# Kernel optimization log

Measured on AMD Instinct MI355X. Metric: run time of the kernel, lower is better.

The kernel has to match this reference:

```python
import jax, jax.numpy as jnp
import numpy as np
import math

P = 2; GS = 64; TPS = 32; T = TPS * TPS; DIM = 256; NH = 8; HD = DIM // NH; NL = 5; FFH = 1024
SCALES = ((0.15, 16), (0.3, 32))
ENC_H = 32; ENC_O = 64
XMIN, XMAX, YMIN, YMAX = -2.0, 4.0, -1.5, 1.5
NFREQ = 10
N_PTS = 20000; N_Q = 100000; G = GS * GS


def rope_tables():
    half = HD // 2
    inv = 1.0 / (10000.0 ** (jnp.arange(0, half, 2, dtype=jnp.float32) / half))  # [HD/4]
    h = jnp.arange(TPS, dtype=jnp.float32)
    w = jnp.arange(TPS, dtype=jnp.float32)
    hg, wg = jnp.meshgrid(h, w, indexing='ij')
    ax = wg.reshape(-1)[:, None] * inv[None, :]  # [T, HD/4]
    ay = hg.reshape(-1)[:, None] * inv[None, :]
    return jnp.cos(ax), jnp.sin(ax), jnp.cos(ay), jnp.sin(ay)


def apply_rope(x, cx, sx, cy, sy):
    B, H, Tn, D = x.shape
    hd = D // 2; pd = hd // 2
    xp = x[..., :hd].reshape(B, H, Tn, pd, 2)
    yp = x[..., hd:].reshape(B, H, Tn, pd, 2)
    cx = cx[None, None]; sx = sx[None, None]; cy = cy[None, None]; sy = sy[None, None]
    rx = jnp.stack([xp[..., 0] * cx - xp[..., 1] * sx, xp[..., 0] * sx + xp[..., 1] * cx], -1).reshape(B, H, Tn, hd)
    ry = jnp.stack([yp[..., 0] * cy - yp[..., 1] * sy, yp[..., 0] * sy + yp[..., 1] * cy], -1).reshape(B, H, Tn, hd)
    return jnp.concatenate([rx, ry], -1)


def rmsnorm(x, w):
    n = jax.lax.rsqrt(jnp.mean(x.astype(jnp.float32) ** 2, -1, keepdims=True) + 1e-6)
    return (x.astype(jnp.float32) * n).astype(x.dtype) * w


def encode_scale(grid, points, radius, k, w1, b1, w2, b2):
    # squared distances [G, N] via gemm (monotone in euclidean dist -> same topk)
    g2 = jnp.sum(grid ** 2, -1, keepdims=True)
    p2 = jnp.sum(points ** 2, -1)
    d2 = g2 + p2[None, :] - 2.0 * (grid @ points.T)
    neg, idx = jax.lax.top_k(-d2, k)  # k nearest
    valid = (-neg) < radius * radius  # [G, k]
    rel = points[idx] - grid[:, None, :]  # [G, k, 2]
    rel = jnp.where(valid[..., None], rel, 0.0)
    h = jax.nn.relu(rel @ w1 + b1)
    f = h @ w2 + b2  # [G, k, ENC_O]
    masked = jnp.where(valid[..., None], f, -jnp.inf)
    pooled = jnp.max(masked, axis=1)
    return jnp.where(jnp.any(valid, axis=1)[:, None], pooled, 0.0)


def fourier_feats(x):
    freqs = (2.0 ** jnp.arange(NFREQ, dtype=jnp.float32)) * math.pi
    scaled = x[..., None] * freqs  # [..., 2, NFREQ]
    enc = jnp.concatenate([jnp.sin(scaled), jnp.cos(scaled)], -1).reshape(*x.shape[:-1], -1)
    return jnp.concatenate([x, enc], -1)  # [..., 2*(1+2*NFREQ)]


def bilinear_sample(feat, xn, yn):
    # feat [C,H,W]; xn,yn in [-1,1]; align_corners=True, border padding
    C, H, W = feat.shape
    px = (xn + 1.0) * 0.5 * (W - 1)
    py = (yn + 1.0) * 0.5 * (H - 1)
    x0 = jnp.clip(jnp.floor(px), 0, W - 1)
    y0 = jnp.clip(jnp.floor(py), 0, H - 1)
    wx = px - x0; wy = py - y0
    x0i = x0.astype(jnp.int32); y0i = y0.astype(jnp.int32)
    x1i = jnp.clip(x0i + 1, 0, W - 1); y1i = jnp.clip(y0i + 1, 0, H - 1)
    f00 = feat[:, y0i, x0i]; f01 = feat[:, y0i, x1i]
    f10 = feat[:, y1i, x0i]; f11 = feat[:, y1i, x1i]
    out = (f00 * (1 - wx) * (1 - wy) + f01 * wx * (1 - wy) + f10 * (1 - wx) * wy + f11 * wx * wy)
    return out.T  # [N, C]


def forward(points, grid, query_pos, query_uinf, query_sdf, query_sdf_grad,
            enc_w1, enc_b1, enc_w2, enc_b2, inproj_w, inproj_b, patch_w, patch_b,
            norm1_w, qkv_w, attnproj_w, norm2_w, gate_w, value_w, ffnout_w,
            unpatch_w, unpatch_b, posmlp_w1, posmlp_b1, posmlp_w2, posmlp_b2,
            pred_w1, pred_b1, pred_w2, pred_b2):
    # --- PointNet multi-scale encoder onto grid ---
    feats = [encode_scale(grid, points, SCALES[i][0], SCALES[i][1],
                          enc_w1[i], enc_b1[i], enc_w2[i], enc_b2[i]) for i in range(len(SCALES))]
    gfeat = jnp.concatenate(feats, -1) @ inproj_w + inproj_b  # [G, DIM]
    img = gfeat.reshape(GS, GS, DIM).transpose(2, 0, 1)[None]  # [1, DIM, GS, GS]
    # --- patchify ---
    x = img.reshape(1, DIM, TPS, P, TPS, P).transpose(0, 2, 4, 1, 3, 5).reshape(1, T, DIM * P * P)
    tok = x @ patch_w + patch_b  # [1, T, DIM]
    cx, sx, cy, sy = rope_tables()
    scale = 1.0 / math.sqrt(HD)
    for l in range(NL):
        h = rmsnorm(tok, norm1_w[l])
        qkv = (h @ qkv_w[l]).reshape(1, T, 3, NH, HD).transpose(2, 0, 3, 1, 4)
        q, k, v = qkv[0], qkv[1], qkv[2]
        q = apply_rope(q, cx, sx, cy, sy)
        k = apply_rope(k, cx, sx, cy, sy)
        att = jax.nn.softmax(jnp.einsum('bhqd,bhkd->bhqk', q, k) * scale, axis=-1)
        o = jnp.einsum('bhqk,bhkd->bhqd', att, v).transpose(0, 2, 1, 3).reshape(1, T, DIM)
        tok = tok + o @ attnproj_w[l]
        h2 = rmsnorm(tok, norm2_w[l])
        tok = tok + (jax.nn.silu(h2 @ gate_w[l]) * (h2 @ value_w[l])) @ ffnout_w[l]
    up = tok @ unpatch_w + unpatch_b  # [1, T, DIM*P*P]
    proc = up.reshape(1, TPS, TPS, DIM, P, P).transpose(0, 3, 1, 4, 2, 5).reshape(1, DIM, GS, GS)
    # --- decoder ---
    xn = jnp.clip(2.0 * (query_pos[:, 0] - XMIN) / (XMAX - XMIN) - 1.0, -1.0, 1.0)
    yn = jnp.clip(2.0 * (query_pos[:, 1] - YMIN) / (YMAX - YMIN) - 1.0, -1.0, 1.0)
    local = bilinear_sample(proc[0], xn, yn)  # [Nq, DIM]
    fp = fourier_feats(jnp.stack([xn, yn], -1))  # [Nq, 42]
    other = jnp.concatenate([query_uinf, query_sdf, query_sdf_grad], -1)  # [Nq, 5]
    pin = jnp.concatenate([fp, other], -1)  # [Nq, 47]
    pe = jax.nn.relu(pin @ posmlp_w1 + posmlp_b1) @ posmlp_w2 + posmlp_b2  # [Nq, 512]
    ctx = jnp.concatenate([local, pe], -1)  # [Nq, 768]
    return jax.nn.relu(ctx @ pred_w1 + pred_b1) @ pred_w2 + pred_b2  # [Nq, 4]


def setup_inputs() -> dict:
    key = jax.random.key(0)
    ks = jax.random.split(key, 32)
    def lin(k, fi, fo, stack=None):
        sh = (fi, fo) if stack is None else (stack, fi, fo)
        return jax.random.normal(k, sh, jnp.float32) / np.sqrt(fi)
    ux = jax.random.uniform(ks[0], (N_PTS, 2), jnp.float32)
    points = jnp.stack([XMIN + ux[:, 0] * (XMAX - XMIN), YMIN + ux[:, 1] * (YMAX - YMIN)], -1)
    gx = jnp.linspace(XMIN, XMAX, GS); gy = jnp.linspace(YMIN, YMAX, GS)
    gyy, gxx = jnp.meshgrid(gy, gx, indexing='ij')
    grid = jnp.stack([gxx.reshape(-1), gyy.reshape(-1)], -1).astype(jnp.float32)  # row-major (H,W)
    uq = jax.random.uniform(ks[1], (N_Q, 2), jnp.float32)
    query_pos = jnp.stack([XMIN + uq[:, 0] * (XMAX - XMIN), YMIN + uq[:, 1] * (YMAX - YMIN)], -1)
    nsc = len(SCALES); pf = DIM * P * P; cdim = 2 * (1 + 2 * NFREQ) + 5
    return {
        'points': points, 'grid': grid, 'query_pos': query_pos,
        'query_uinf': jax.random.normal(ks[2], (N_Q, 2), jnp.float32),
        'query_sdf': jax.random.normal(ks[3], (N_Q, 1), jnp.float32),
        'query_sdf_grad': jax.random.normal(ks[4], (N_Q, 2), jnp.float32),
        'enc_w1': lin(ks[5], 2, ENC_H, nsc), 'enc_b1': jnp.zeros((nsc, ENC_H), jnp.float32),
        'enc_w2': lin(ks[6], ENC_H, ENC_O, nsc), 'enc_b2': jnp.zeros((nsc, ENC_O), jnp.float32),
        'inproj_w': lin(ks[7], ENC_O * nsc, DIM), 'inproj_b': jnp.zeros((DIM,), jnp.float32),
        'patch_w': lin(ks[8], pf, DIM), 'patch_b': jnp.zeros((DIM,), jnp.float32),
        'norm1_w': jnp.ones((NL, DIM), jnp.float32),
        'qkv_w': lin(ks[9], DIM, 3 * DIM, NL),
        'attnproj_w': lin(ks[10], DIM, DIM, NL),
        'norm2_w': jnp.ones((NL, DIM), jnp.float32),
        'gate_w': lin(ks[11], DIM, FFH, NL),
        'value_w': lin(ks[12], DIM, FFH, NL),
        'ffnout_w': lin(ks[13], FFH, DIM, NL),
        'unpatch_w': lin(ks[14], DIM, pf), 'unpatch_b': jnp.zeros((pf,), jnp.float32),
        'posmlp_w1': lin(ks[15], cdim, 256), 'posmlp_b1': jnp.zeros((256,), jnp.float32),
        'posmlp_w2': lin(ks[16], 256, 512), 'posmlp_b2': jnp.zeros((512,), jnp.float32),
        'pred_w1': lin(ks[17], DIM + 512, 256), 'pred_b1': jnp.zeros((256,), jnp.float32),
        'pred_w2': lin(ks[18], 256, 4), 'pred_b2': jnp.zeros((4,), jnp.float32),
    }


def reference(points, grid, query_pos, query_uinf, query_sdf, query_sdf_grad,
              enc_w1, enc_b1, enc_w2, enc_b2, inproj_w, inproj_b, patch_w, patch_b,
              norm1_w, qkv_w, attnproj_w, norm2_w, gate_w, value_w, ffnout_w,
              unpatch_w, unpatch_b, posmlp_w1, posmlp_b1, posmlp_w2, posmlp_b2,
              pred_w1, pred_b1, pred_w2, pred_b2):
    return forward(points, grid, query_pos, query_uinf, query_sdf, query_sdf_grad,
                   enc_w1, enc_b1, enc_w2, enc_b2, inproj_w, inproj_b, patch_w, patch_b,
                   norm1_w, qkv_w, attnproj_w, norm2_w, gate_w, value_w, ffnout_w,
                   unpatch_w, unpatch_b, posmlp_w1, posmlp_b1, posmlp_w2, posmlp_b2,
                   pred_w1, pred_b1, pred_w2, pred_b2)
```

## Files before the change

### kernel.cpp

```cpp
#include <hip/hip_runtime.h>
#include <math.h>

typedef __attribute__((ext_vector_type(8))) short short8;
typedef __attribute__((ext_vector_type(8))) unsigned short ushort8;
typedef __attribute__((ext_vector_type(4))) unsigned short ushort4v;
typedef __attribute__((ext_vector_type(4))) float f32x4;
typedef __attribute__((ext_vector_type(16))) float f32x16;

#define NPTS  20000
#define NQ    100000
#define TOK   1024
#define DIMD  256
#define NHD   8
#define NLAY  5
#define GRD   4096
#define CAP   512
#define QN    32

#define XMINF (-2.0f)
#define YMINF (-1.5f)
#define CELL  0.15f
#define NCX   40
#define NCY   20
#define NCELL 800
// ... 133 lines not shown
    if (pi < nsel) {
      float rx = s_selx[pi] - gx;
      float ry = s_sely[pi] - gy;
      float f = B2[d];
      #pragma unroll
      for (int j = 0; j < 32; ++j) {
        float h = rx * W1[j] + ry * W1[32 + j] + B1[j];
        h = fmaxf(h, 0.0f);
        f += h * W2[j*64 + d];
      }
      s_part[grp][d] = fmaxf(s_part[grp][d], f);
    }
  }
  __syncthreads();
  if (tid < 64) {
    float v = fmaxf(fmaxf(s_part[0][tid], s_part[1][tid]),
                    fmaxf(s_part[2][tid], s_part[3][tid]));
    if (nsel == 0) v = 0.0f;
    ushort h, l; split2(v, h, l);
    fH[gi*128 + sc*64 + tid] = h;
    fL[gi*128 + sc*64 + tid] = l;
  }
}

__global__ void k_gemm(const float* __restrict__ A, const float* __restrict__ B,
                       float* __restrict__ C, int M, int N, int K) {
  __shared__ float As[32][33];
  __shared__ float Bs[32][33];
  int bm = blockIdx.y * 32, bn = blockIdx.x * 32;
  int tx = threadIdx.x & 31, ty = threadIdx.x >> 5;
  float acc[4] = {0.f, 0.f, 0.f, 0.f};
  for (int k0 = 0; k0 < K; k0 += 32) {
    for (int i = threadIdx.x; i < 1024; i += 256) {
      int r = i >> 5, c = i & 31;
      As[r][c] = A[(size_t)(bm + r)*K + k0 + c];
      Bs[r][c] = B[(size_t)(k0 + r)*N + bn + c];
    }
    __syncthreads();
    #pragma unroll
    for (int kk = 0; kk < 32; ++kk) {
      float bv = Bs[kk][tx];
      #pragma unroll
      for (int i = 0; i < 4; ++i) acc[i] += As[ty + 8*i][kk] * bv;
    }
    __syncthreads();
  }
  #pragma unroll
  for (int i = 0; i < 4; ++i)
    C[(size_t)(bm + ty + 8*i)*N + bn + tx] = acc[i];
}

__global__ void k_beff(const float* __restrict__ db1, const float* __restrict__ pb2,
                       const float* __restrict__ dw1, float* __restrict__ b2eff) {
  int n = threadIdx.x;
  float a = db1[n];
  for (int j = 0; j < 512; ++j) a += pb2[j] * dw1[(size_t)(256 + j)*256 + n];
  b2eff[n] = a;
}

struct SDesc { const float* src; ushort* dh; ushort* dl; int K, N, Kp, blk0; };
struct STable { int nw; SDesc d[31]; };

__global__ void k_splitT_all(STable tab) {
  __shared__ float tile[32][33];
  int b = blockIdx.x;
  int w = 0;
  for (int i = 1; i < tab.nw; ++i) if (b >= tab.d[i].blk0) w = i;
  SDesc s = tab.d[w];
  int rel = b - s.blk0;
  int ntn = s.N >> 5;
  int tk = rel / ntn, tn = rel - tk*ntn;
  int r = threadIdx.x >> 5, c = threadIdx.x & 31;
  #pragma unroll
  for (int i = 0; i < 4; ++i) {
    int kk = tk*32 + r + i*8;
    tile[r + i*8][c] = (kk < s.K) ? s.src[(size_t)kk*s.N + tn*32 + c] : 0.f;
  }
  __syncthreads();
  #pragma unroll
  for (int i = 0; i < 4; ++i) {
    int nn = tn*32 + r + i*8;
    float v = tile[c][r + i*8];
    ushort hh, ll; split2(v, hh, ll);
    size_t o = (size_t)nn*s.Kp + tk*32 + c;
    s.dh[o] = hh; s.dl[o] = ll;
  }
}

template<bool BIAS, bool RESID, bool WSPLIT>
__global__ __launch_bounds__(256,2)
void k_mgemm64(const ushort* __restrict__ Ah, const ushort* __restrict__ Al,
               const ushort* __restrict__ Bh, const ushort* __restrict__ Bl,
               const float* __restrict__ bias, const float* __restrict__ resid,
               float* __restrict__ C, int M, int N, int K,
               ushort* __restrict__ wsH, ushort* __restrict__ wsL) {
  __shared__ ushort sAh[64*40], sAl[64*40], sBh[64*40], sBl[64*40];
  int tid = threadIdx.x;
  int wave = tid >> 6, lane = tid & 63, l15 = lane & 15, lhi = lane >> 4;
  int bm = blockIdx.y * 64, bn = blockIdx.x * 64;
  int sr = tid >> 2, sg = (tid & 3) * 8;
  const size_t aoff = (size_t)(bm + sr) * K + sg;
  const size_t boff = (size_t)(bn + sr) * K + sg;
  f32x4 acc[4];
  #pragma unroll
  for (int m = 0; m < 4; ++m) acc[m] = (f32x4){0.f,0.f,0.f,0.f};

  for (int k0 = 0; k0 < K; k0 += 32) {
    __syncthreads();
    *(ushort8*)(sAh + sr*40 + sg) = *(const ushort8*)(Ah + aoff + k0);
    *(ushort8*)(sAl + sr*40 + sg) = *(const ushort8*)(Al + aoff + k0);
// ... 110 lines not shown
  int sr = tid >> 2, sg = (tid & 3) * 8;
  const int K = 256;
  const size_t aoff = (size_t)(bm + sr) * K + sg;
  const size_t boff = (size_t)(bn + sr) * K + sg;
  f32x4 acc[4];
  #pragma unroll
  for (int m = 0; m < 4; ++m) acc[m] = (f32x4){0.f,0.f,0.f,0.f};

  for (int k0 = 0; k0 < K; k0 += 32) {
    __syncthreads();
    *(ushort8*)(sAh + sr*40 + sg) = *(const ushort8*)(Ah + aoff + k0);
    *(ushort8*)(sAl + sr*40 + sg) = *(const ushort8*)(Al + aoff + k0);
    *(ushort8*)(sBh + sr*40 + sg) = *(const ushort8*)(Bh + boff + k0);
    *(ushort8*)(sBl + sr*40 + sg) = *(const ushort8*)(Bl + boff + k0);
    __syncthreads();
    short8 ah[4], al[4];
    #pragma unroll
    for (int m = 0; m < 4; ++m) {
      int r = m*16 + l15;
      ah[m] = *(const short8*)(sAh + r*40 + lhi*8);
      al[m] = *(const short8*)(sAl + r*40 + lhi*8);
    }
    int rb = wave*16 + l15;
    short8 bh = *(const short8*)(sBh + rb*40 + lhi*8);
    short8 bl = *(const short8*)(sBl + rb*40 + lhi*8);
    #pragma unroll
    for (int m = 0; m < 4; ++m) {
      acc[m] = MFMA(ah[m], bh, acc[m]);
      acc[m] = MFMA(al[m], bh, acc[m]);
      acc[m] = MFMA(ah[m], bl, acc[m]);
    }
  }

  int u = bn + wave*16 + l15;
  float bv = bias[u];
  int c  = u >> 2;
  int py = (u >> 1) & 1, px = u & 1;
  #pragma unroll
  for (int m = 0; m < 4; ++m) {
    int gr0 = bm + m*16 + lhi*4;
    #pragma unroll
    for (int r = 0; r < 4; ++r) {
      int t = gr0 + r;
      int y = (t >> 5)*2 + py, x = (t & 31)*2 + px;
      float v = acc[m][r] + bv;
      ushort hh, ll; split2(v, hh, ll);
      size_t o = (size_t)(y*64 + x)*256 + c;
      pH[o] = hh; pL[o] = ll;
    }
  }
}

__global__ __launch_bounds__(256,2)
void k_qkvrope(const ushort* __restrict__ Ah, const ushort* __restrict__ Al,
               const ushort* __restrict__ Bh, const ushort* __restrict__ Bl,
               ushort* __restrict__ QsH, ushort* __restrict__ QsL,
               ushort* __restrict__ KsH, ushort* __restrict__ KsL,
               ushort* __restrict__ VtH, ushort* __restrict__ VtL) {
  __shared__ ushort sAh[64*40], sAl[64*40], sBh[64*40], sBl[64*40];
  int tid = threadIdx.x;
  int wave = tid >> 6, lane = tid & 63, l15 = lane & 15, lhi = lane >> 4;
  int bm = blockIdx.y * 64, bn = blockIdx.x * 64;
  int sr = tid >> 2, sg = (tid & 3) * 8;
  const int K = 256, N = 768;
  const size_t aoff = (size_t)(bm + sr) * K + sg;
  const size_t boff = (size_t)(bn + sr) * K + sg;
  f32x4 acc[4];
  #pragma unroll
  for (int m = 0; m < 4; ++m) acc[m] = (f32x4){0.f,0.f,0.f,0.f};
  (void)N;

  for (int k0 = 0; k0 < K; k0 += 32) {
    __syncthreads();
    *(ushort8*)(sAh + sr*40 + sg) = *(const ushort8*)(Ah + aoff + k0);
    *(ushort8*)(sAl + sr*40 + sg) = *(const ushort8*)(Al + aoff + k0);
    *(ushort8*)(sBh + sr*40 + sg) = *(const ushort8*)(Bh + boff + k0);
    *(ushort8*)(sBl + sr*40 + sg) = *(const ushort8*)(Bl + boff + k0);
    __syncthreads();
    short8 ah[4], al[4];
    #pragma unroll
    for (int m = 0; m < 4; ++m) {
      int r = m*16 + l15;
      ah[m] = *(const short8*)(sAh + r*40 + lhi*8);
      al[m] = *(const short8*)(sAl + r*40 + lhi*8);
    }
    int rb = wave*16 + l15;
    short8 bh = *(const short8*)(sBh + rb*40 + lhi*8);
    short8 bl = *(const short8*)(sBl + rb*40 + lhi*8);
    #pragma unroll
    for (int m = 0; m < 4; ++m) {
      acc[m] = MFMA(ah[m], bh, acc[m]);
      acc[m] = MFMA(al[m], bh, acc[m]);
      acc[m] = MFMA(ah[m], bl, acc[m]);
    }
  }

  int gc = bn + wave*16 + l15;
  if (gc < 512) {
    int qk = gc >> 8;
    int c  = gc & 255;
    int h  = c >> 5, d = c & 31;
    int half = d >> 4, dd = d & 15, pd = dd >> 1, odd = dd & 1;
    float inv = powf(10.0f, -0.5f * (float)pd);
    float scl = qk ? 1.0f : 0.17677669529663687f;
    ushort* dH = qk ? KsH : QsH;
    ushort* dL = qk ? KsL : QsL;
    #pragma unroll
    for (int m = 0; m < 4; ++m) {
      int gr0 = bm + m*16 + lhi*4;
      #pragma unroll
      for (int r = 0; r < 4; ++r) {
        int t = gr0 + r;
        float v = acc[m][r];
        float pv = __shfl_xor(v, 1);
        float pos = (float)(half ? (t >> 5) : (t & 31));
        float ang = pos * inv;
        float cs = __cosf(ang), sn = __sinf(ang);
        float res = odd ? (pv*sn + v*cs) : (v*cs - pv*sn);
        res *= scl;
        ushort hh, ll; split2(res, hh, ll);
        size_t o = (size_t)h*32768 + (size_t)t*32 + d;
        dH[o] = hh; dL[o] = ll;
      }
    }
  } else {
    int c = gc - 512;
    int h = c >> 5, d = c & 31;
    #pragma unroll
    for (int m = 0; m < 4; ++m) {
      int t0 = bm + m*16 + lhi*4;
      ushort4v vh, vl;
      #pragma unroll
      for (int r = 0; r < 4; ++r) {
        ushort hh, ll; split2(acc[m][r], hh, ll);
        vh[r] = hh; vl[r] = ll;
      }
      size_t o = (size_t)h*32768 + (size_t)d*1024 + t0;
      *(ushort4v*)(VtH + o) = vh;
      *(ushort4v*)(VtL + o) = vl;
    }
  }
}

__global__ void k_rmsnorm_split(const float* __restrict__ x, const float* __restrict__ w,
                                ushort* __restrict__ yH, ushort* __restrict__ yL) {
  __shared__ float red[256];
  int row = blockIdx.x, t = threadIdx.x;
  float v = x[(size_t)row*DIMD + t];
  red[t] = v * v;
  __syncthreads();
  for (int off = 128; off; off >>= 1) {
    if (t < off) red[t] += red[t + off];
    __syncthreads();
  }
  float n = 1.0f / sqrtf(red[0] / 256.0f + 1e-6f);
  float y = v * n * w[t];
  ushort h, l; split2(y, h, l);
  yH[(size_t)row*DIMD + t] = h;
  yL[(size_t)row*DIMD + t] = l;
}

__global__ __launch_bounds__(512,1)
void k_fattn(const ushort* __restrict__ QsH, const ushort* __restrict__ QsL,
             const ushort* __restrict__ KsH, const ushort* __restrict__ KsL,
             const ushort* __restrict__ VtH, const ushort* __restrict__ VtL,
             ushort* __restrict__ oH, ushort* __restrict__ oL) {
  __shared__ float sM[8][64], sL[8][64];
  __shared__ float sO[8][64][16];
  int h  = blockIdx.x >> 5;
  int qt = blockIdx.x & 31;
  int tid = threadIdx.x;
  int wv = tid >> 6, lane = tid & 63;
  int l31 = lane & 31, lhi = (lane >> 5) & 1;

  const size_t qoff = ((size_t)h*1024 + qt*32 + l31)*32 + lhi*8;
  short8 qh = *(const short8*)(QsH + qoff);
  short8 ql = *(const short8*)(QsL + qoff);

  f32x16 oacc;
  #pragma unroll
  for (int r = 0; r < 16; ++r) oacc[r] = 0.f;
  float mrun = -INFINITY, lrun = 0.f;

  for (int kt = wv*4; kt < wv*4 + 4; ++kt) {
    const size_t koff = ((size_t)h*1024 + kt*32 + l31)*32 + lhi*8;
    short8 kh = *(const short8*)(KsH + koff);
    short8 kl = *(const short8*)(KsL + koff);
    const size_t voff = ((size_t)h*32 + l31)*1024 + kt*32 + lhi*8;
    short8 vh0 = *(const short8*)(VtH + voff);
    short8 vl0 = *(const short8*)(VtL + voff);
    short8 vh1 = *(const short8*)(VtH + voff + 16);
    short8 vl1 = *(const short8*)(VtL + voff + 16);

    f32x16 s;
    #pragma unroll
    for (int r = 0; r < 16; ++r) s[r] = 0.f;
    s = MFMA32(kh, qh, s);
    s = MFMA32(kl, qh, s);
    s = MFMA32(kh, ql, s);

    float mloc = s[0];
    #pragma unroll
    for (int r = 1; r < 16; ++r) mloc = fmaxf(mloc, s[r]);
    mloc = fmaxf(mloc, __shfl_xor(mloc, 32));
    float mnew = fmaxf(mrun, mloc);
    float fsc = __expf(mrun - mnew);
    float p[16]; float ssum = 0.f;
    #pragma unroll
    for (int r = 0; r < 16; ++r) { p[r] = __expf(s[r] - mnew); ssum += p[r]; }
    ssum += __shfl_xor(ssum, 32);
    lrun = lrun * fsc + ssum;
    mrun = mnew;
    #pragma unroll
    for (int r = 0; r < 16; ++r) oacc[r] *= fsc;
// ... 17 lines not shown
    U bh0, bl0, bh1, bl1;
    bh0.u[0] = lhi ? pwh[2] : wh[0];  bh0.u[1] = lhi ? pwh[3] : wh[1];
    bh0.u[2] = lhi ? wh[2]  : pwh[0]; bh0.u[3] = lhi ? wh[3]  : pwh[1];
    bl0.u[0] = lhi ? pwl[2] : wl[0];  bl0.u[1] = lhi ? pwl[3] : wl[1];
    bl0.u[2] = lhi ? wl[2]  : pwl[0]; bl0.u[3] = lhi ? wl[3]  : pwl[1];
    bh1.u[0] = lhi ? pwh[6] : wh[4];  bh1.u[1] = lhi ? pwh[7] : wh[5];
    bh1.u[2] = lhi ? wh[6]  : pwh[4]; bh1.u[3] = lhi ? wh[7]  : pwh[5];
    bl1.u[0] = lhi ? pwl[6] : wl[4];  bl1.u[1] = lhi ? pwl[7] : wl[5];
    bl1.u[2] = lhi ? wl[6]  : pwl[4]; bl1.u[3] = lhi ? wl[7]  : pwl[5];

    oacc = MFMA32(vh0, bh0.s, oacc);
    oacc = MFMA32(vl0, bh0.s, oacc);
    oacc = MFMA32(vh0, bl0.s, oacc);
    oacc = MFMA32(vh1, bh1.s, oacc);
    oacc = MFMA32(vl1, bh1.s, oacc);
    oacc = MFMA32(vh1, bl1.s, oacc);
  }

  sM[wv][lane] = mrun;
  sL[wv][lane] = lrun;
  #pragma unroll
  for (int r = 0; r < 16; ++r) sO[wv][lane][r] = oacc[r];
  __syncthreads();

  if (wv == 0) {
    float M = sM[0][lane];
    #pragma unroll
    for (int w = 1; w < 8; ++w) M = fmaxf(M, sM[w][lane]);
    float L = 0.f;
    float O[16];
    #pragma unroll
    for (int r = 0; r < 16; ++r) O[r] = 0.f;
    #pragma unroll
    for (int w = 0; w < 8; ++w) {
      float f = __expf(sM[w][lane] - M);
      L += sL[w][lane] * f;
      #pragma unroll
      for (int r = 0; r < 16; ++r) O[r] += sO[w][lane][r] * f;
    }
    float inv = 1.0f / L;
    int t = qt*32 + l31;
    #pragma unroll
    for (int r = 0; r < 16; ++r) {
      int d = (r & 3) + 8*(r >> 2) + 4*lhi;
      float v = O[r] * inv;
      ushort hh, ll; split2(v, hh, ll);
      oH[(size_t)t*DIMD + h*32 + d] = hh;
      oL[(size_t)t*DIMD + h*32 + d] = ll;
    }
  }
}

__global__ __launch_bounds__(256,2)
void k_ffgv(const ushort* __restrict__ Ah, const ushort* __restrict__ Al,
            const ushort* __restrict__ Bh, const ushort* __restrict__ Bl,
            ushort* __restrict__ fH, ushort* __restrict__ fL) {
  __shared__ ushort sAh[64*40], sAl[64*40];
  __shared__ ushort sGh[64*40], sGl[64*40];
  __shared__ ushort sVh[64*40], sVl[64*40];
  int tid = threadIdx.x;
  int wave = tid >> 6, lane = tid & 63, l15 = lane & 15, lhi = lane >> 4;
  int bm = blockIdx.y * 64, bn = blockIdx.x * 64;
  int sr = tid >> 2, sg = (tid & 3) * 8;
  const size_t aoff = (size_t)(bm + sr) * 256 + sg;
  const size_t goff = (size_t)(bn + sr) * 256 + sg;
  const size_t voff = (size_t)(1024 + bn + sr) * 256 + sg;
  f32x4 accg[4], accv[4];
  #pragma unroll
  for (int m = 0; m < 4; ++m) { accg[m] = (f32x4){0.f,0.f,0.f,0.f}; accv[m] = accg[m]; }

  for (int k0 = 0; k0 < 256; k0 += 32) {
    __syncthreads();
    *(ushort8*)(sAh + sr*40 + sg) = *(const ushort8*)(Ah + aoff + k0);
    *(ushort8*)(sAl + sr*40 + sg) = *(const ushort8*)(Al + aoff + k0);
    *(ushort8*)(sGh + sr*40 + sg) = *(const ushort8*)(Bh + goff + k0);
    *(ushort8*)(sGl + sr*40 + sg) = *(const ushort8*)(Bl + goff + k0);
    *(ushort8*)(sVh + sr*40 + sg) = *(const ushort8*)(Bh + voff + k0);
    *(ushort8*)(sVl + sr*40 + sg) = *(const ushort8*)(Bl + voff + k0);
    __syncthreads();
    short8 ah[4], al[4];
    #pragma unroll
    for (int m = 0; m < 4; ++m) {
      int r = m*16 + l15;
      ah[m] = *(const short8*)(sAh + r*40 + lhi*8);
      al[m] = *(const short8*)(sAl + r*40 + lhi*8);
    }
    int rb = wave*16 + l15;
    short8 gh = *(const short8*)(sGh + rb*40 + lhi*8);
    short8 gl = *(const short8*)(sGl + rb*40 + lhi*8);
    short8 vh = *(const short8*)(sVh + rb*40 + lhi*8);
    short8 vl = *(const short8*)(sVl + rb*40 + lhi*8);
    #pragma unroll
    for (int m = 0; m < 4; ++m) {
      accg[m] = MFMA(ah[m], gh, accg[m]);
      accg[m] = MFMA(al[m], gh, accg[m]);
      accg[m] = MFMA(ah[m], gl, accg[m]);
      accv[m] = MFMA(ah[m], vh, accv[m]);
      accv[m] = MFMA(al[m], vh, accv[m]);
      accv[m] = MFMA(ah[m], vl, accv[m]);
    }
  }

  int gc = bn + wave*16 + l15;
  #pragma unroll
  for (int m = 0; m < 4; ++m) {
    int gr0 = bm + m*16 + lhi*4;
    #pragma unroll
    for (int r = 0; r < 4; ++r) {
      float g = accg[m][r], v = accv[m][r];
      float s = g / (1.0f + expf(-g));
      float rr = s * v;
      ushort hh, ll; split2(rr, hh, ll);
      size_t idx = (size_t)(gr0 + r)*1024 + gc;
      fH[idx] = hh; fL[idx] = ll;
    }
  }
}

__global__ __launch_bounds__(512,4)
void k_qhead(const float* __restrict__ qpos, const float* __restrict__ quinf,
             const float* __restrict__ qsdf, const float* __restrict__ qgrad,
             const float* __restrict__ projCL,
             const ushort* __restrict__ pw1tH, const ushort* __restrict__ pw1tL,
             const float* __restrict__ pb1,
             const ushort* __restrict__ wcH, const ushort* __restrict__ wcL,
             const float* __restrict__ b2eff,
             const float* __restrict__ dw2, const float* __restrict__ db2,
             float* __restrict__ out) {
  __shared__ ushort sPinH[QN*72], sPinL[QN*72];
  __shared__ ushort sH1H[QN*264], sH1L[QN*264];
  __shared__ float  sXY[QN][2];
  __shared__ float  sRed[8][128];

  int tid = threadIdx.x;
  int w = tid >> 6, lane = tid & 63, l15 = lane & 15, lhi = lane >> 4;
  int q0 = blockIdx.x * QN;

  if (tid < QN) {
    int qg = q0 + tid;
    float x = qpos[(size_t)qg*2 + 0], y = qpos[(size_t)qg*2 + 1];
    float xn = fminf(fmaxf(2.0f*(x + 2.0f)/6.0f - 1.0f, -1.0f), 1.0f);
    float yn = fminf(fmaxf(2.0f*(y + 1.5f)/3.0f - 1.0f, -1.0f), 1.0f);
    sXY[tid][0] = xn; sXY[tid][1] = yn;
  }
  __syncthreads();

  {
    int q = tid >> 4;
    int j0 = (tid & 15) * 4;
    int qg = q0 + q;
    float xn = sXY[q][0], yn = sXY[q][1];
    #pragma unroll
    for (int jj = 0; jj < 4; ++jj) {
      int j = j0 + jj;
      float v = 0.f;
      if (j == 0) v = xn;
      else if (j == 1) v = yn;
      else if (j < 42) {
        int z = j - 2;
        int coord = z / 20;
        int ww = z % 20;
        int isCos = ww / 10;
        int fi = ww % 10;
        float f = ldexpf(3.14159265358979323846f, fi);
        float a = (coord ? yn : xn) * f;
        v = isCos ? __cosf(a) : __sinf(a);
      }
      else if (j < 44) v = quinf[(size_t)qg*2 + (j-42)];
      else if (j == 44) v = qsdf[qg];
      else if (j < 47) v = qgrad[(size_t)qg*2 + (j-45)];
      ushort h, l; split2(v, h, l);
      sPinH[q*72 + j] = h; sPinL[q*72 + j] = l;
    }
  }
  __syncthreads();

  f32x4 acc[2][2];
  #pragma unroll
  for (int m = 0; m < 2; ++m)
    #pragma unroll
    for (int n = 0; n < 2; ++n) acc[m][n] = (f32x4){0.f,0.f,0.f,0.f};

  #pragma unroll
  for (int ks = 0; ks < 2; ++ks) {
    short8 bh[2], bl[2];
    #pragma unroll
    for (int n = 0; n < 2; ++n) {
      int r = w*32 + n*16 + l15;
      bh[n] = *(const short8*)(pw1tH + r*64 + ks*32 + lhi*8);
      bl[n] = *(const short8*)(pw1tL + r*64 + ks*32 + lhi*8);
    }
    short8 ah[2], al[2];
    #pragma unroll
    for (int m = 0; m < 2; ++m) {
      int r = m*16 + l15;
      ah[m] = *(const short8*)(sPinH + r*72 + ks*32 + lhi*8);
      al[m] = *(const short8*)(sPinL + r*72 + ks*32 + lhi*8);
    }
    #pragma unroll
    for (int m = 0; m < 2; ++m)
      #pragma unroll
      for (int n = 0; n < 2; ++n) {
        acc[m][n] = MFMA(ah[m], bh[n], acc[m][n]);
        acc[m][n] = MFMA(al[m], bh[n], acc[m][n]);
        acc[m][n] = MFMA(ah[m], bl[n], acc[m][n]);
      }
  }
  #pragma unroll
  for (int m = 0; m < 2; ++m) {
    #pragma unroll
    for (int n = 0; n < 2; ++n) {
      int col = w*32 + n*16 + l15;
      float bv = pb1[col];
      #pragma unroll
      for (int r = 0; r < 4; ++r) {
        int row = m*16 + lhi*4 + r;
        float v = fmaxf(acc[m][n][r] + bv, 0.f);
        ushort h, l; split2(v, h, l);
        sH1H[row*264 + col] = h;
        sH1L[row*264 + col] = l;
      }
      acc[m][n] = (f32x4){0.f,0.f,0.f,0.f};
    }
  }
  __syncthreads();

  #pragma unroll
  for (int ks = 0; ks < 8; ++ks) {
    short8 bh[2], bl[2];
    #pragma unroll
    for (int n = 0; n < 2; ++n) {
      int r = w*32 + n*16 + l15;
      bh[n] = *(const short8*)(wcH + (size_t)r*256 + ks*32 + lhi*8);
      bl[n] = *(const short8*)(wcL + (size_t)r*256 + ks*32 + lhi*8);
    }
    short8 ah[2], al[2];
    #pragma unroll
    for (int m = 0; m < 2; ++m) {
      int r = m*16 + l15;
      ah[m] = *(const short8*)(sH1H + r*264 + ks*32 + lhi*8);
      al[m] = *(const short8*)(sH1L + r*264 + ks*32 + lhi*8);
    }
    #pragma unroll
    for (int m = 0; m < 2; ++m)
      #pragma unroll
      for (int n = 0; n < 2; ++n) {
        acc[m][n] = MFMA(ah[m], bh[n], acc[m][n]);
        acc[m][n] = MFMA(al[m], bh[n], acc[m][n]);
        acc[m][n] = MFMA(ah[m], bl[n], acc[m][n]);
      }
  }

  float part[2][4][4];
  #pragma unroll
  for (int m = 0; m < 2; ++m)
    #pragma unroll
    for (int r = 0; r < 4; ++r)
      #pragma unroll
      for (int d = 0; d < 4; ++d) part[m][r][d] = 0.f;

  #pragma unroll
  for (int m = 0; m < 2; ++m) {
    #pragma unroll
    for (int r = 0; r < 4; ++r) {
      int q = m*16 + lhi*4 + r;
      float xn = sXY[q][0], yn = sXY[q][1];
      float px = (xn + 1.0f) * 0.5f * 63.0f;
      float py = (yn + 1.0f) * 0.5f * 63.0f;
      float x0 = fminf(fmaxf(floorf(px), 0.f), 63.f);
      float y0 = fminf(fmaxf(floorf(py), 0.f), 63.f);
      float wx = px - x0, wy = py - y0;
      int x0i = (int)x0, y0i = (int)y0;
      int x1i = min(x0i + 1, 63), y1i = min(y0i + 1, 63);
      const float* p00 = projCL + (size_t)(y0i*64 + x0i)*256;
      const float* p01 = projCL + (size_t)(y0i*64 + x1i)*256;
      const float* p10 = projCL + (size_t)(y1i*64 + x0i)*256;
      const float* p11 = projCL + (size_t)(y1i*64 + x1i)*256;
      float w00 = (1.f-wx)*(1.f-wy), w01 = wx*(1.f-wy), w10 = (1.f-wx)*wy, w11 = wx*wy;
      #pragma unroll
      for (int n = 0; n < 2; ++n) {
        int col = w*32 + n*16 + l15;
        float bil = w00*p00[col] + w01*p01[col] + w10*p10[col] + w11*p11[col];
        float v = fmaxf(acc[m][n][r] + b2eff[col] + bil, 0.f);
        f32x4 wv = *(const f32x4*)(dw2 + col*4);
        part[m][r][0] += v * wv[0];
        part[m][r][1] += v * wv[1];
        part[m][r][2] += v * wv[2];
        part[m][r][3] += v * wv[3];
      }
    }
  }

  #pragma unroll
  for (int bit = 1; bit <= 8; bit <<= 1) {
    #pragma unroll
    for (int m = 0; m < 2; ++m)
      #pragma unroll
      for (int r = 0; r < 4; ++r)
        #pragma unroll
        for (int d = 0; d < 4; ++d)
          part[m][r][d] += __shfl_xor(part[m][r][d], bit);
  }
  if (l15 == 0) {
    #pragma unroll
    for (int m = 0; m < 2; ++m)
      #pragma unroll
      for (int r = 0; r < 4; ++r)
        #pragma unroll
        for (int d = 0; d < 4; ++d)
          sRed[w][((lhi*2 + m)*4 + r)*4 + d] = part[m][r][d];
  }
  __syncthreads();

  if (tid < 128) {
    int q = tid >> 2, d = tid & 3;
    int m = q >> 4, lh = (q >> 2) & 3, r = q & 3;
    int idx = ((lh*2 + m)*4 + r)*4 + d;
    float a = db2[d];
    #pragma unroll
    for (int ww = 0; ww < 8; ++ww) a += sRed[ww][idx];
    out[(size_t)(q0 + q)*4 + d] = a;
  }
}

extern "C" void kernel_launch(void* const* d_in, const int* in_sizes, int n_in,
                              void* d_out, int out_size, void* d_ws, size_t ws_size,
                              hipStream_t stream) {
  (void)in_sizes; (void)n_in; (void)out_size; (void)ws_size;
  const float* points     = (const float*)d_in[0];
  const float* grd        = (const float*)d_in[1];
  const float* qpos       = (const float*)d_in[2];
  const float* quinf      = (const float*)d_in[3];
  const float* qsdf       = (const float*)d_in[4];
  const float* qgrad      = (const float*)d_in[5];
  const float* enc_w1     = (const float*)d_in[6];
  const float* enc_b1     = (const float*)d_in[7];
  const float* enc_w2     = (const float*)d_in[8];
  const float* enc_b2     = (const float*)d_in[9];
  const float* inproj_w   = (const float*)d_in[10];
  const float* inproj_b   = (const float*)d_in[11];
  const float* patch_w    = (const float*)d_in[12];
  const float* patch_b    = (const float*)d_in[13];
  const float* norm1_w    = (const float*)d_in[14];
  const float* qkv_w      = (const float*)d_in[15];
  const float* attnproj_w = (const float*)d_in[16];
  const float* norm2_w    = (const float*)d_in[17];
  const float* gate_w     = (const float*)d_in[18];
  const float* value_w    = (const float*)d_in[19];
  const float* ffnout_w   = (const float*)d_in[20];
  const float* unpatch_w  = (const float*)d_in[21];
  const float* unpatch_b  = (const float*)d_in[22];
  const float* pw1        = (const float*)d_in[23];
  const float* pb1        = (const float*)d_in[24];
  const float* pw2        = (const float*)d_in[25];
  const float* pb2        = (const float*)d_in[26];
  const float* dw1        = (const float*)d_in[27];
  const float* db1        = (const float*)d_in[28];
  const float* dw2        = (const float*)d_in[29];
  const float* db2        = (const float*)d_in[30];
  float* out = (float*)d_out;

  char* base = (char*)d_ws;
  size_t off = 0;
  auto alloc = [&](size_t bytes) -> void* {
    void* p = base + off; off += (bytes + 255) & ~(size_t)255; return p;
  };

  ushort* inprojTH = (ushort*)alloc(32768*2);   ushort* inprojTL = (ushort*)alloc(32768*2);
  ushort* patchTH  = (ushort*)alloc(262144*2);  ushort* patchTL  = (ushort*)alloc(262144*2);
  ushort* upTH     = (ushort*)alloc(262144*2);  ushort* upTL     = (ushort*)alloc(262144*2);
  ushort* pw1TH    = (ushort*)alloc(16384*2);   ushort* pw1TL    = (ushort*)alloc(16384*2);
  ushort* wcTH     = (ushort*)alloc(65536*2);   ushort* wcTL     = (ushort*)alloc(65536*2);
  ushort* dw1aTH   = (ushort*)alloc(65536*2);   ushort* dw1aTL   = (ushort*)alloc(65536*2);
  float*  Wcomb    = (float*)alloc(65536*4);
  float*  b2eff    = (float*)alloc(256*4);

  int*   cellcnt   = (int*)alloc(NCELL*4);
  int*   cellstart = (int*)alloc((NCELL+1)*4);
  int*   cursor    = (int*)alloc(NCELL*4);
  float* bpx       = (float*)alloc(NPTS*4);
  float* bpy       = (float*)alloc(NPTS*4);
  int*   bpi       = (int*)alloc(NPTS*4);

  ushort* lwH = (ushort*)alloc((size_t)NLAY*1048576*2);
  ushort* lwL = (ushort*)alloc((size_t)NLAY*1048576*2);
  const size_t qkvO = 0, apO = 196608, gateO = 262144, foO = 786432;

  ushort* featcH = (ushort*)alloc(524288*2);   ushort* featcL = (ushort*)alloc(524288*2);
  ushort* xpH = (ushort*)alloc(1048576*2);
  ushort* xpL = (ushort*)alloc(1048576*2);
  float*  tok = (float*)alloc(262144*4);
  ushort* hH  = (ushort*)alloc(262144*2);
  ushort* hL  = (ushort*)alloc(262144*2);
  ushort* oH  = (ushort*)alloc(262144*2);
  ushort* oL  = (ushort*)alloc(262144*2);
  float*  unionBuf = (float*)alloc(2097152*4);
  float*  projCL = unionBuf + 1048576;

  ushort* QsH = (ushort*)unionBuf;
  ushort* QsL = QsH + 262144;
  ushort* KsH = QsH + 2*262144;
  ushort* KsL = QsH + 3*262144;
  ushort* VtH = QsH + 4*262144;
  ushort* VtL = QsH + 5*262144;

  ushort* ffH = xpH;  ushort* ffL = xpL;
  ushort* prH = xpH;  ushort* prL = xpL;
  ushort* tkH = hH;   ushort* tkL = hL;

  k_gemm<<<dim3(8,8), 256, 0, stream>>>(pw2, dw1 + 256*256, Wcomb, 256, 256, 512);
  k_beff<<<1, 256, 0, stream>>>(db1, pb2, dw1, b2eff);

  auto addw = [](STable& t, int& cb, const float* src, ushort* dh, ushort* dl,
                 int K, int N, int Kp) {
    SDesc& s = t.d[t.nw]; s.src = src; s.dh = dh; s.dl = dl;
    s.K = K; s.N = N; s.Kp = Kp; s.blk0 = cb;
    cb += (Kp >> 5) * (N >> 5); t.nw++;
  };

  {
    STable gt; gt.nw = 0; int cb = 0;
    addw(gt, cb, inproj_w, inprojTH, inprojTL, 128, 256, 128);
    addw(gt, cb, patch_w,  patchTH,  patchTL,  1024, 256, 1024);
    addw(gt, cb, unpatch_w, upTH, upTL, 256, 1024, 256);
    addw(gt, cb, pw1,   pw1TH,  pw1TL,  47, 256, 64);
    addw(gt, cb, Wcomb, wcTH,   wcTL,   256, 256, 256);
    addw(gt, cb, dw1,   dw1aTH, dw1aTL, 256, 256, 256);
    for (int l = 0; l < NLAY; ++l) {
      size_t lb = (size_t)l*1048576;
      addw(gt, cb, qkv_w      + (size_t)l*196608, lwH + lb + qkvO,  lwL + lb + qkvO,  256, 768, 256);
      addw(gt, cb, attnproj_w + (size_t)l*65536,  lwH + lb + apO,   lwL + lb + apO,   256, 256, 256);
      addw(gt, cb, gate_w     + (size_t)l*262144, lwH + lb + gateO,          lwL + lb + gateO,          256, 1024, 256);
      addw(gt, cb, value_w    + (size_t)l*262144, lwH + lb + gateO + 262144, lwL + lb + gateO + 262144, 256, 1024, 256);
      addw(gt, cb, ffnout_w   + (size_t)l*262144, lwH + lb + foO,   lwL + lb + foO,   1024, 256, 1024);
    }
    k_splitT_all<<<cb, 256, 0, stream>>>(gt);
  }

  k_zero<<<4, 256, 0, stream>>>(cellcnt);
  k_bincount<<<(NPTS+255)/256, 256, 0, stream>>>(points, cellcnt);
  k_prefix<<<1, 1024, 0, stream>>>(cellcnt, cellstart, cursor);
  k_scatter<<<(NPTS+255)/256, 256, 0, stream>>>(points, cursor, bpx, bpy, bpi);

  k_encode<<<dim3(GRD, 2), 256, 0, stream>>>(bpx, bpy, bpi, cellstart, grd,
                                             enc_w1, enc_b1, enc_w2, enc_b2, featcH, featcL);
  k_inproj<<<dim3(4,64), 256, 0, stream>>>(featcH, featcL, inprojTH, inprojTL, inproj_b, xpH, xpL);
  k_mgemm64<true,false,false><<<dim3(4,16), 256, 0, stream>>>(xpH, xpL, patchTH, patchTL, patch_b, nullptr, tok, TOK, 256, 1024, nullptr, nullptr);

  for (int l = 0; l < NLAY; ++l) {
    size_t lb = (size_t)l*1048576;
    k_rmsnorm_split<<<TOK, 256, 0, stream>>>(tok, norm1_w + (size_t)l*DIMD, hH, hL);
    k_qkvrope<<<dim3(12,16), 256, 0, stream>>>(hH, hL, lwH + lb + qkvO, lwL + lb + qkvO,
                                               QsH, QsL, KsH, KsL, VtH, VtL);
    k_fattn<<<256, 512, 0, stream>>>(QsH, QsL, KsH, KsL, VtH, VtL, oH, oL);
    k_mgemm64<false,true,false><<<dim3(4,16), 256, 0, stream>>>(oH, oL, lwH + lb + apO, lwL + lb + apO, nullptr, tok, tok, TOK, 256, 256, nullptr, nullptr);
    k_rmsnorm_split<<<TOK, 256, 0, stream>>>(tok, norm2_w + (size_t)l*DIMD, hH, hL);
    k_ffgv<<<dim3(16,16), 256, 0, stream>>>(hH, hL, lwH + lb + gateO, lwL + lb + gateO, ffH, ffL);
    if (l < NLAY-1)
      k_mgemm64<false,true,false><<<dim3(4,16), 256, 0, stream>>>(ffH, ffL, lwH + lb + foO, lwL + lb + foO, nullptr, tok, tok, TOK, 256, 1024, nullptr, nullptr);
    else
      k_mgemm64<false,true,true><<<dim3(4,16), 256, 0, stream>>>(ffH, ffL, lwH + lb + foO, lwL + lb + foO, nullptr, tok, tok, TOK, 256, 1024, tkH, tkL);
  }

  k_upgemm<<<dim3(16,16), 256, 0, stream>>>(tkH, tkL, upTH, upTL, unpatch_b, prH, prL);
  k_mgemm64<false,false,false><<<dim3(4,64), 256, 0, stream>>>(prH, prL, dw1aTH, dw1aTL, nullptr, nullptr, projCL, GRD, 256, 256, nullptr, nullptr);

  k_qhead<<<NQ/QN, 512, 0, stream>>>(qpos, quinf, qsdf, qgrad, projCL,
      pw1TH, pw1TL, pb1, wcTH, wcTL, b2eff, dw2, db2, out);
}
```

Before: 740.1 us.

## Fuse RMSNorm into QKV and FFN GEMMs, MFMA final head projection

Removes the standalone rmsnorm kernels by computing per-row norms inside the QKV and gate/value GEMM blocks and normalizing/splitting A tiles on load. This saves 10 launches and the intermediate hi/lo buffers, but each column block recomputes the row norms. The query head's final 256→4 projection now runs as a padded MFMA over a pre-split transposed dw2 instead of scalar FMAs plus shuffle reductions, and the combined-weight B fragments are register-prefetched. k_beff is parallelized across 8 blocks and k_qhead launch bounds raised to 5 waves per EU, which may cost registers.

```diff
diff --git a/kernel.cpp b/kernel.cpp
--- a/kernel.cpp
+++ b/kernel.cpp
@@ -209,10 +209,32 @@
 
 __global__ void k_beff(const float* __restrict__ db1, const float* __restrict__ pb2,
                        const float* __restrict__ dw1, float* __restrict__ b2eff) {
-  int n = threadIdx.x;
-  float a = db1[n];
-  for (int j = 0; j < 512; ++j) a += pb2[j] * dw1[(size_t)(256 + j)*256 + n];
-  b2eff[n] = a;
+  __shared__ float red[8][32];
+  int n0 = blockIdx.x * 32;
+  int t = threadIdx.x;
+  int nn = t & 31, jc = t >> 5;
+  float a = 0.f;
+  for (int j = jc*64; j < jc*64 + 64; ++j)
+    a += pb2[j] * dw1[(size_t)(256 + j)*256 + n0 + nn];
+  red[jc][nn] = a;
+  __syncthreads();
+  if (t < 32) {
+    float s = db1[n0 + t];
+    #pragma unroll
+    for (int w = 0; w < 8; ++w) s += red[w][t];
+    b2eff[n0 + t] = s;
+  }
+}
+
+__global__ void k_dw2t(const float* __restrict__ dw2,
+                       ushort* __restrict__ tH, ushort* __restrict__ tL) {
+  int k = threadIdx.x;
+  #pragma unroll
+  for (int d = 0; d < 16; ++d) {
+    float v = (d < 4) ? dw2[k*4 + d] : 0.f;
+    ushort h, l; split2(v, h, l);
+    tH[d*256 + k] = h; tL[d*256 + k] = l;
+  }
 }
 
 struct SDesc { const float* src; ushort* dh; ushort* dl; int K, N, Kp, blk0; };
@@ -429,28 +451,56 @@
 }
 
 __global__ __launch_bounds__(256,2)
-void k_qkvrope(const ushort* __restrict__ Ah, const ushort* __restrict__ Al,
+void k_qkvrope(const float* __restrict__ tok, const float* __restrict__ nw,
                const ushort* __restrict__ Bh, const ushort* __restrict__ Bl,
                ushort* __restrict__ QsH, ushort* __restrict__ QsL,
                ushort* __restrict__ KsH, ushort* __restrict__ KsL,
                ushort* __restrict__ VtH, ushort* __restrict__ VtL) {
   __shared__ ushort sAh[64*40], sAl[64*40], sBh[64*40], sBl[64*40];
+  __shared__ float sp[64][4];
+  __shared__ float snorm[64];
+  __shared__ float swt[256];
   int tid = threadIdx.x;
   int wave = tid >> 6, lane = tid & 63, l15 = lane & 15, lhi = lane >> 4;
   int bm = blockIdx.y * 64, bn = blockIdx.x * 64;
   int sr = tid >> 2, sg = (tid & 3) * 8;
-  const int K = 256, N = 768;
-  const size_t aoff = (size_t)(bm + sr) * K + sg;
+  const int K = 256;
   const size_t boff = (size_t)(bn + sr) * K + sg;
+
+  swt[tid] = nw[tid];
+  {
+    int r = tid >> 2, p = tid & 3;
+    const float* row = tok + (size_t)(bm + r)*256 + p*64;
+    float s = 0.f;
+    for (int j = 0; j < 64; j += 4) {
+      f32x4 v = *(const f32x4*)(row + j);
+      s += v[0]*v[0] + v[1]*v[1] + v[2]*v[2] + v[3]*v[3];
+    }
+    sp[r][p] = s;
+  }
+  __syncthreads();
+  if (tid < 64)
+    snorm[tid] = rsqrtf((sp[tid][0]+sp[tid][1]+sp[tid][2]+sp[tid][3]) * (1.0f/256.0f) + 1e-6f);
+
   f32x4 acc[4];
   #pragma unroll
   for (int m = 0; m < 4; ++m) acc[m] = (f32x4){0.f,0.f,0.f,0.f};
-  (void)N;
 
   for (int k0 = 0; k0 < K; k0 += 32) {
     __syncthreads();
-    *(ushort8*)(sAh + sr*40 + sg) = *(const ushort8*)(Ah + aoff + k0);
-    *(ushort8*)(sAl + sr*40 + sg) = *(const ushort8*)(Al + aoff + k0);
+    {
+      float nrm = snorm[sr];
+      const float* src = tok + (size_t)(bm + sr)*256 + k0 + sg;
+      ushort8 vh, vl;
+      #pragma unroll
+      for (int j = 0; j < 8; ++j) {
+        float v = src[j] * nrm * swt[k0 + sg + j];
+        ushort hh, ll; split2(v, hh, ll);
+        vh[j] = hh; vl[j] = ll;
+      }
+      *(ushort8*)(sAh + sr*40 + sg) = vh;
+      *(ushort8*)(sAl + sr*40 + sg) = vl;
+    }
     *(ushort8*)(sBh + sr*40 + sg) = *(const ushort8*)(Bh + boff + k0);
     *(ushort8*)(sBl + sr*40 + sg) = *(const ushort8*)(Bl + boff + k0);
     __syncthreads();
@@ -519,24 +569,6 @@
   }
 }
 
-__global__ void k_rmsnorm_split(const float* __restrict__ x, const float* __restrict__ w,
-                                ushort* __restrict__ yH, ushort* __restrict__ yL) {
-  __shared__ float red[256];
-  int row = blockIdx.x, t = threadIdx.x;
-  float v = x[(size_t)row*DIMD + t];
-  red[t] = v * v;
-  __syncthreads();
-  for (int off = 128; off; off >>= 1) {
-    if (t < off) red[t] += red[t + off];
-    __syncthreads();
-  }
-  float n = 1.0f / sqrtf(red[0] / 256.0f + 1e-6f);
-  float y = v * n * w[t];
-  ushort h, l; split2(y, h, l);
-  yH[(size_t)row*DIMD + t] = h;
-  yL[(size_t)row*DIMD + t] = l;
-}
-
 __global__ __launch_bounds__(512,1)
 void k_fattn(const ushort* __restrict__ QsH, const ushort* __restrict__ QsL,
              const ushort* __restrict__ KsH, const ushort* __restrict__ KsL,
@@ -660,27 +692,56 @@
 }
 
 __global__ __launch_bounds__(256,2)
-void k_ffgv(const ushort* __restrict__ Ah, const ushort* __restrict__ Al,
+void k_ffgv(const float* __restrict__ tok, const float* __restrict__ nw,
             const ushort* __restrict__ Bh, const ushort* __restrict__ Bl,
             ushort* __restrict__ fH, ushort* __restrict__ fL) {
   __shared__ ushort sAh[64*40], sAl[64*40];
   __shared__ ushort sGh[64*40], sGl[64*40];
   __shared__ ushort sVh[64*40], sVl[64*40];
+  __shared__ float sp[64][4];
+  __shared__ float snorm[64];
+  __shared__ float swt[256];
   int tid = threadIdx.x;
   int wave = tid >> 6, lane = tid & 63, l15 = lane & 15, lhi = lane >> 4;
   int bm = blockIdx.y * 64, bn = blockIdx.x * 64;
   int sr = tid >> 2, sg = (tid & 3) * 8;
-  const size_t aoff = (size_t)(bm + sr) * 256 + sg;
   const size_t goff = (size_t)(bn + sr) * 256 + sg;
   const size_t voff = (size_t)(1024 + bn + sr) * 256 + sg;
+
+  swt[tid] = nw[tid];
+  {
+    int r = tid >> 2, p = tid & 3;
+    const float* row = tok + (size_t)(bm + r)*256 + p*64;
+    float s = 0.f;
+    for (int j = 0; j < 64; j += 4) {
+      f32x4 v = *(const f32x4*)(row + j);
+      s += v[0]*v[0] + v[1]*v[1] + v[2]*v[2] + v[3]*v[3];
+    }
+    sp[r][p] = s;
+  }
+  __syncthreads();
+  if (tid < 64)
+    snorm[tid] = rsqrtf((sp[tid][0]+sp[tid][1]+sp[tid][2]+sp[tid][3]) * (1.0f/256.0f) + 1e-6f);
+
   f32x4 accg[4], accv[4];
   #pragma unroll
   for (int m = 0; m < 4; ++m) { accg[m] = (f32x4){0.f,0.f,0.f,0.f}; accv[m] = accg[m]; }
 
   for (int k0 = 0; k0 < 256; k0 += 32) {
     __syncthreads();
-    *(ushort8*)(sAh + sr*40 + sg) = *(const ushort8*)(Ah + aoff + k0);
-    *(ushort8*)(sAl + sr*40 + sg) = *(const ushort8*)(Al + aoff + k0);
+    {
+      float nrm = snorm[sr];
+      const float* src = tok + (size_t)(bm + sr)*256 + k0 + sg;
+      ushort8 vh, vl;
+      #pragma unroll
+      for (int j = 0; j < 8; ++j) {
+        float v = src[j] * nrm * swt[k0 + sg + j];
+        ushort hh, ll; split2(v, hh, ll);
+        vh[j] = hh; vl[j] = ll;
+      }
+      *(ushort8*)(sAh + sr*40 + sg) = vh;
+      *(ushort8*)(sAl + sr*40 + sg) = vl;
+    }
     *(ushort8*)(sGh + sr*40 + sg) = *(const ushort8*)(Bh + goff + k0);
     *(ushort8*)(sGl + sr*40 + sg) = *(const ushort8*)(Bl + goff + k0);
     *(ushort8*)(sVh + sr*40 + sg) = *(const ushort8*)(Bh + voff + k0);
@@ -725,7 +786,7 @@
   }
 }
 
-__global__ __launch_bounds__(512,4)
+__global__ __launch_bounds__(512,5)
 void k_qhead(const float* __restrict__ qpos, const float* __restrict__ quinf,
              const float* __restrict__ qsdf, const float* __restrict__ qgrad,
              const float* __restrict__ projCL,
@@ -733,7 +794,8 @@
              const float* __restrict__ pb1,
              const ushort* __restrict__ wcH, const ushort* __restrict__ wcL,
              const float* __restrict__ b2eff,
-             const float* __restrict__ dw2, const float* __restrict__ db2,
+             const ushort* __restrict__ dw2tH, const ushort* __restrict__ dw2tL,
+             const float* __restrict__ db2,
              float* __restrict__ out) {
   __shared__ ushort sPinH[QN*72], sPinL[QN*72];
   __shared__ ushort sH1H[QN*264], sH1L[QN*264];
@@ -833,14 +895,25 @@
   }
   __syncthreads();
 
+  short8 pbh[2], pbl[2];
+  #pragma unroll
+  for (int n = 0; n < 2; ++n) {
+    int r = w*32 + n*16 + l15;
+    pbh[n] = *(const short8*)(wcH + (size_t)r*256 + lhi*8);
+    pbl[n] = *(const short8*)(wcL + (size_t)r*256 + lhi*8);
+  }
   #pragma unroll
   for (int ks = 0; ks < 8; ++ks) {
     short8 bh[2], bl[2];
     #pragma unroll
-    for (int n = 0; n < 2; ++n) {
-      int r = w*32 + n*16 + l15;
-      bh[n] = *(const short8*)(wcH + (size_t)r*256 + ks*32 + lhi*8);
-      bl[n] = *(const short8*)(wcL + (size_t)r*256 + ks*32 + lhi*8);
+    for (int n = 0; n < 2; ++n) { bh[n] = pbh[n]; bl[n] = pbl[n]; }
+    if (ks < 7) {
+      #pragma unroll
+      for (int n = 0; n < 2; ++n) {
+        int r = w*32 + n*16 + l15;
+        pbh[n] = *(const short8*)(wcH + (size_t)r*256 + (ks+1)*32 + lhi*8);
+        pbl[n] = *(const short8*)(wcL + (size_t)r*256 + (ks+1)*32 + lhi*8);
+      }
     }
     short8 ah[2], al[2];
     #pragma unroll
@@ -858,14 +931,7 @@
         acc[m][n] = MFMA(ah[m], bl[n], acc[m][n]);
       }
   }
-
-  float part[2][4][4];
-  #pragma unroll
-  for (int m = 0; m < 2; ++m)
-    #pragma unroll
-    for (int r = 0; r < 4; ++r)
-      #pragma unroll
-      for (int d = 0; d < 4; ++d) part[m][r][d] = 0.f;
+  __syncthreads();
 
   #pragma unroll
   for (int m = 0; m < 2; ++m) {
@@ -890,43 +956,47 @@
         int col = w*32 + n*16 + l15;
         float bil = w00*p00[col] + w01*p01[col] + w10*p10[col] + w11*p11[col];
         float v = fmaxf(acc[m][n][r] + b2eff[col] + bil, 0.f);
-        f32x4 wv = *(const f32x4*)(dw2 + col*4);
-        part[m][r][0] += v * wv[0];
-        part[m][r][1] += v * wv[1];
-        part[m][r][2] += v * wv[2];
-        part[m][r][3] += v * wv[3];
-      }
-    }
-  }
-
-  #pragma unroll
-  for (int bit = 1; bit <= 8; bit <<= 1) {
-    #pragma unroll
-    for (int m = 0; m < 2; ++m)
-      #pragma unroll
-      for (int r = 0; r < 4; ++r)
+        ushort hh, ll; split2(v, hh, ll);
+        sH1H[q*264 + col] = hh;
+        sH1L[q*264 + col] = ll;
+      }
+    }
+  }
+  __syncthreads();
+
+  {
+    short8 ah2[2], al2[2];
+    #pragma unroll
+    for (int m = 0; m < 2; ++m) {
+      int r = m*16 + l15;
+      ah2[m] = *(const short8*)(sH1H + r*264 + w*32 + lhi*8);
+      al2[m] = *(const short8*)(sH1L + r*264 + w*32 + lhi*8);
+    }
+    short8 bh2 = *(const short8*)(dw2tH + (size_t)l15*256 + w*32 + lhi*8);
+    short8 bl2 = *(const short8*)(dw2tL + (size_t)l15*256 + w*32 + lhi*8);
+    f32x4 c[2];
+    #pragma unroll
+    for (int m = 0; m < 2; ++m) {
+      c[m] = (f32x4){0.f,0.f,0.f,0.f};
+      c[m] = MFMA(ah2[m], bh2, c[m]);
+      c[m] = MFMA(al2[m], bh2, c[m]);
+      c[m] = MFMA(ah2[m], bl2, c[m]);
+    }
+    if (l15 < 4) {
+      #pragma unroll
+      for (int m = 0; m < 2; ++m)
         #pragma unroll
-        for (int d = 0; d < 4; ++d)
-          part[m][r][d] += __shfl_xor(part[m][r][d], bit);
-  }
-  if (l15 == 0) {
-    #pragma unroll
-    for (int m = 0; m < 2; ++m)
-      #pragma unroll
-      for (int r = 0; r < 4; ++r)
-        #pragma unroll
-        for (int d = 0; d < 4; ++d)
-          sRed[w][((lhi*2 + m)*4 + r)*4 + d] = part[m][r][d];
+        for (int r = 0; r < 4; ++r)
+          sRed[w][(m*16 + lhi*4 + r)*4 + l15] = c[m][r];
+    }
   }
   __syncthreads();
 
   if (tid < 128) {
     int q = tid >> 2, d = tid & 3;
-    int m = q >> 4, lh = (q >> 2) & 3, r = q & 3;
-    int idx = ((lh*2 + m)*4 + r)*4 + d;
     float a = db2[d];
     #pragma unroll
-    for (int ww = 0; ww < 8; ++ww) a += sRed[ww][idx];
+    for (int ww = 0; ww < 8; ++ww) a += sRed[ww][q*4 + d];
     out[(size_t)(q0 + q)*4 + d] = a;
   }
 }
@@ -980,6 +1050,7 @@
   ushort* pw1TH    = (ushort*)alloc(16384*2);   ushort* pw1TL    = (ushort*)alloc(16384*2);
   ushort* wcTH     = (ushort*)alloc(65536*2);   ushort* wcTL     = (ushort*)alloc(65536*2);
   ushort* dw1aTH   = (ushort*)alloc(65536*2);   ushort* dw1aTL   = (ushort*)alloc(65536*2);
+  ushort* dw2tH    = (ushort*)alloc(4096*2);    ushort* dw2tL    = (ushort*)alloc(4096*2);
   float*  Wcomb    = (float*)alloc(65536*4);
   float*  b2eff    = (float*)alloc(256*4);
 
@@ -998,8 +1069,8 @@
   ushort* xpH = (ushort*)alloc(1048576*2);
   ushort* xpL = (ushort*)alloc(1048576*2);
   float*  tok = (float*)alloc(262144*4);
-  ushort* hH  = (ushort*)alloc(262144*2);
-  ushort* hL  = (ushort*)alloc(262144*2);
+  ushort* tkH = (ushort*)alloc(262144*2);
+  ushort* tkL = (ushort*)alloc(262144*2);
   ushort* oH  = (ushort*)alloc(262144*2);
   ushort* oL  = (ushort*)alloc(262144*2);
   float*  unionBuf = (float*)alloc(2097152*4);
@@ -1014,10 +1085,10 @@
 
   ushort* ffH = xpH;  ushort* ffL = xpL;
   ushort* prH = xpH;  ushort* prL = xpL;
-  ushort* tkH = hH;   ushort* tkL = hL;
 
   k_gemm<<<dim3(8,8), 256, 0, stream>>>(pw2, dw1 + 256*256, Wcomb, 256, 256, 512);
-  k_beff<<<1, 256, 0, stream>>>(db1, pb2, dw1, b2eff);
+  k_beff<<<8, 256, 0, stream>>>(db1, pb2, dw1, b2eff);
+  k_dw2t<<<1, 256, 0, stream>>>(dw2, dw2tH, dw2tL);
 
   auto addw = [](STable& t, int& cb, const float* src, ushort* dh, ushort* dl,
                  int K, int N, int Kp) {
@@ -1057,13 +1128,13 @@
 
   for (int l = 0; l < NLAY; ++l) {
     size_t lb = (size_t)l*1048576;
-    k_rmsnorm_split<<<TOK, 256, 0, stream>>>(tok, norm1_w + (size_t)l*DIMD, hH, hL);
-    k_qkvrope<<<dim3(12,16), 256, 0, stream>>>(hH, hL, lwH + lb + qkvO, lwL + lb + qkvO,
+    k_qkvrope<<<dim3(12,16), 256, 0, stream>>>(tok, norm1_w + (size_t)l*DIMD,
+                                               lwH + lb + qkvO, lwL + lb + qkvO,
                                                QsH, QsL, KsH, KsL, VtH, VtL);
     k_fattn<<<256, 512, 0, stream>>>(QsH, QsL, KsH, KsL, VtH, VtL, oH, oL);
     k_mgemm64<false,true,false><<<dim3(4,16), 256, 0, stream>>>(oH, oL, lwH + lb + apO, lwL + lb + apO, nullptr, tok, tok, TOK, 256, 256, nullptr, nullptr);
-    k_rmsnorm_split<<<TOK, 256, 0, stream>>>(tok, norm2_w + (size_t)l*DIMD, hH, hL);
-    k_ffgv<<<dim3(16,16), 256, 0, stream>>>(hH, hL, lwH + lb + gateO, lwL + lb + gateO, ffH, ffL);
+    k_ffgv<<<dim3(16,16), 256, 0, stream>>>(tok, norm2_w + (size_t)l*DIMD,
+                                            lwH + lb + gateO, lwL + lb + gateO, ffH, ffL);
     if (l < NLAY-1)
       k_mgemm64<false,true,false><<<dim3(4,16), 256, 0, stream>>>(ffH, ffL, lwH + lb + foO, lwL + lb + foO, nullptr, tok, tok, TOK, 256, 1024, nullptr, nullptr);
     else
@@ -1074,5 +1145,5 @@
   k_mgemm64<false,false,false><<<dim3(4,64), 256, 0, stream>>>(prH, prL, dw1aTH, dw1aTL, nullptr, nullptr, projCL, GRD, 256, 256, nullptr, nullptr);
 
   k_qhead<<<NQ/QN, 512, 0, stream>>>(qpos, quinf, qsdf, qgrad, projCL,
-      pw1TH, pw1TL, pb1, wcTH, wcTL, b2eff, dw2, db2, out);
-}
+      pw1TH, pw1TL, pb1, wcTH, wcTL, b2eff, dw2tH, dw2tL, db2, out);
+}
```

New measurement: 714.0 us. -3.5%, faster.
